# Kernel tuning notes

Hardware: AMD Instinct MI355X
Metric: run time of the kernel (lower is better)

The kernel has to match this reference:

```python
import jax, jax.numpy as jnp
import numpy as np

B = 4096
D_IN = 1024
HIDDEN = [1024, 512, 256]
NUM_DOMAINS = 8


def _glorot(key, shape):
    fan_in, fan_out = shape[-2], shape[-1]
    std = np.sqrt(2.0 / (fan_in + fan_out)).astype(np.float32)
    return jax.random.normal(key, shape, dtype=jnp.float32) * std


def setup_inputs() -> dict:
    key = jax.random.key(0)
    keys = jax.random.split(key, 16)
    dims = [D_IN] + HIDDEN  # per-layer (in, out) = (dims[i], dims[i+1])
    inp = {
        "x": jax.random.normal(keys[0], (B, D_IN), dtype=jnp.float32),
        "indicator": jax.random.randint(keys[1], (B,), 0, NUM_DOMAINS, dtype=jnp.int32),
    }
    for i in range(len(HIDDEN)):
        inp[f"sk{i}"] = _glorot(keys[2 + i], (dims[i], dims[i + 1]))
        inp[f"sb{i}"] = jnp.zeros((dims[i + 1],), dtype=jnp.float32)
        # per-domain kernels stacked on leading domain axis: (D, in, out)
        inp[f"dk{i}"] = _glorot(keys[6 + i], (NUM_DOMAINS, dims[i], dims[i + 1]))
        inp[f"db{i}"] = jnp.zeros((NUM_DOMAINS, dims[i + 1]), dtype=jnp.float32)
    return inp


def reference(x, indicator, sk0, sb0, dk0, db0, sk1, sb1, dk1, db1, sk2, sb2, dk2, db2):
    shared_k = [sk0, sk1, sk2]
    shared_b = [sb0, sb1, sb2]
    domain_k = [dk0, dk1, dk2]
    domain_b = [db0, db1, db2]
    D = dk0.shape[0]
    # Replicate input across all domains: [B, D, d_in] (source computes every domain stack)
    h = jnp.broadcast_to(x[:, None, :], (x.shape[0], D, x.shape[1]))
    for sk, sb, dk, db in zip(shared_k, shared_b, domain_k, domain_b):
        w_eff = sk[None, :, :] * dk          # [D, in, out]  fused shared*domain weights
        b_eff = sb[None, :] + db             # [D, out]
        h = jnp.einsum('bdi,dio->bdo', h, w_eff) + b_eff[None, :, :]
        h = jax.nn.relu(h)                   # all layers use 'relu' (no output_activation)
    one_hot = jax.nn.one_hot(indicator, D, dtype=h.dtype)  # [B, D]
    return jnp.einsum('bdo,bd->bo', h, one_hot)
```

## Files before the change

kernel.cpp:

```cpp
#include <hip/hip_runtime.h>

#define NROWS 4096
#define NDOM 8

typedef short short8 __attribute__((ext_vector_type(8)));
typedef float floatx4 __attribute__((ext_vector_type(4)));
typedef unsigned short ushort4v __attribute__((ext_vector_type(4)));
typedef unsigned short ushort8v __attribute__((ext_vector_type(8)));

__device__ __forceinline__ unsigned short f2bf(float f) {
    union { float f; unsigned u; } v; v.f = f;
    unsigned r = v.u + 0x7FFFu + ((v.u >> 16) & 1u);
    return (unsigned short)(r >> 16);
}

__device__ __forceinline__ void dma16(const void* g, void* l) {
    __builtin_amdgcn_global_load_lds(
        (const __attribute__((address_space(1))) unsigned*)g,
        (__attribute__((address_space(3))) unsigned*)l, 16, 0, 0);
}

__global__ void bucket_kernel(const int* __restrict__ ind,
                              int* __restrict__ offsets,
                              int* __restrict__ rowidx) {
    __shared__ unsigned short cnt[256][NDOM];
    __shared__ int base[256][NDOM];
    __shared__ int dom_total[NDOM];
    __shared__ int dom_off[NDOM + 1];
    const int t = threadIdx.x;

    int myind[16];
#pragma unroll
    for (int i = 0; i < 16; ++i) myind[i] = ind[t * 16 + i];

    unsigned short c[NDOM];
#pragma unroll
    for (int d = 0; d < NDOM; ++d) c[d] = 0;
#pragma unroll
    for (int i = 0; i < 16; ++i) c[myind[i]]++;
#pragma unroll
    for (int d = 0; d < NDOM; ++d) cnt[t][d] = c[d];
    __syncthreads();

    if (t < NDOM) {
        int acc = 0;
        for (int ch = 0; ch < 256; ++ch) { base[ch][t] = acc; acc += cnt[ch][t]; }
        dom_total[t] = acc;
    }
    __syncthreads();
    if (t == 0) {
        int acc = 0;
        for (int d = 0; d < NDOM; ++d) { dom_off[d] = acc; acc += dom_total[d]; }
        dom_off[NDOM] = acc;
    }
    __syncthreads();

    int pos[NDOM];
#pragma unroll
    for (int d = 0; d < NDOM; ++d) pos[d] = dom_off[d] + base[t][d];
#pragma unroll
    for (int i = 0; i < 16; ++i) {
        int dm = myind[i];
        rowidx[pos[dm]++] = t * 16 + i;
    }
    if (t <= NDOM) offsets[t] = dom_off[t];
}

template <int K, int N>
__device__ __forceinline__ void weff_tile(const float* __restrict__ sk,
                                          const float* __restrict__ dk,
                                          unsigned short* __restrict__ wt,
                                          int local) {
    const int d = local & 7;
    const int rest = local >> 3;
    const int k0 = (rest % (K / 64)) * 64;
    const int n0 = (rest / (K / 64)) * 64;
    const int t = threadIdx.x;
    const int n = n0 + (t & 63);
    const int koff = k0 + (t >> 6) * 16;
    unsigned short wb[16];
#pragma unroll
    for (int kk = 0; kk < 16; ++kk) {
        int k = koff + kk;
        float s = sk[(size_t)k * N + n];
        float dd = dk[((size_t)d * K + k) * N + n];
        wb[kk] = f2bf(s * dd);
    }
    unsigned short* dst = wt + ((size_t)d * N + n) * K + koff;
    *(ushort8v*)dst = *(ushort8v*)wb;
    *(ushort8v*)(dst + 8) = *(ushort8v*)(wb + 8);
}

__global__ void precompute_kernel(const float* __restrict__ x,
                                  const int* __restrict__ rowidx,
                                  const float* __restrict__ sk0, const float* __restrict__ dk0,
                                  const float* __restrict__ sk1, const float* __restrict__ dk1,
                                  const float* __restrict__ sk2, const float* __restrict__ dk2,
                                  unsigned short* __restrict__ xb,
                                  unsigned short* __restrict__ w0t,
                                  unsigned short* __restrict__ w1t,
                                  unsigned short* __restrict__ w2t) {
    const int b = blockIdx.x;
    if (b < 256) {
        const int t = threadIdx.x;
#pragma unroll
        for (int r = 0; r < 16; ++r) {
            int p = b * 16 + r;
            int src = rowidx[p];
            floatx4 v = *(const floatx4*)(x + (size_t)src * 1024 + t * 4);
            ushort4v o;
            o[0] = f2bf(v[0]); o[1] = f2bf(v[1]); o[2] = f2bf(v[2]); o[3] = f2bf(v[3]);
            *(ushort4v*)(xb + (size_t)p * 1024 + t * 4) = o;
        }
    } else if (b < 256 + 2048) {
        weff_tile<1024, 1024>(sk0, dk0, w0t, b - 256);
    } else if (b < 256 + 2048 + 1024) {
        weff_tile<1024, 512>(sk1, dk1, w1t, b - (256 + 2048));
    } else {
        weff_tile<512, 256>(sk2, dk2, w2t, b - (256 + 2048 + 1024));
    }
}

template <int FM, int FN, int MSLOTS, int K, int N, bool SCATTER>
__launch_bounds__(256)
__global__ void star_gemm(const unsigned short* __restrict__ Ab,
                          const unsigned short* __restrict__ Wt,
                          const float* __restrict__ sb,
                          const float* __restrict__ db,
                          float* __restrict__ OutF,
                          unsigned short* __restrict__ OutB,
                          const int* __restrict__ offsets,
                          const int* __restrict__ rowidx) {
    constexpr int BM = 32 * FM;
    constexpr int BN = 32 * FN;
    constexpr int NK = K / 64;
    constexpr int AI = BM / 32;
    constexpr int WI = BN / 32;

    __shared__ __align__(128) unsigned short As[BM * 64];
    __shared__ __align__(128) unsigned short Ws[BN * 64];

    const int gid = blockIdx.x;
    const int d = gid & 7;
    const int mslot = (gid >> 3) % MSLOTS;
    const int n0 = (gid / (8 * MSLOTS)) * BN;

    const int bstart = offsets[d];
    const int bend = offsets[d + 1];
    const int bsize = bend - bstart;

    const int tid = threadIdx.x;
    const int lane = tid & 63;
    const int w = tid >> 6;
    const int wy = w >> 1;
    const int wx = w & 1;
    const int lm = lane & 15;
    const int quad = lane >> 4;

    const int lrow = lane >> 3;
    const int phys = lane & 7;

    float bias[FN];
#pragma unroll
    for (int j = 0; j < FN; ++j) {
        int n = n0 + wx * FN * 16 + j * 16 + lm;
        bias[j] = sb[n] + db[d * N + n];
    }

    const unsigned short* wsrc[WI];
    unsigned short* wdst[WI];
#pragma unroll
    for (int j = 0; j < WI; ++j) {
        int nr0 = (w * WI + j) * 8;
        int nn = nr0 + lrow;
        int ch = phys ^ (nn & 7);
        wsrc[j] = Wt + ((size_t)d * N + n0 + nn) * K + ch * 8;
        wdst[j] = Ws + nr0 * 64;
    }

    for (int mt = mslot; mt * BM < bsize; mt += MSLOTS) {
        const int row_start = bstart + mt * BM;

        const unsigned short* asrc[AI];
        unsigned short* adst[AI];
#pragma unroll
        for (int j = 0; j < AI; ++j) {
            int m0 = (w * AI + j) * 8;
            int mm = m0 + lrow;
            int ch = phys ^ (mm & 7);
            int p = row_start + mm; if (p >= bend) p = bend - 1;
            asrc[j] = Ab + (size_t)p * K + ch * 8;
            adst[j] = As + m0 * 64;
        }

        floatx4 acc[FM][FN];
#pragma unroll
        for (int i = 0; i < FM; ++i)
#pragma unroll
            for (int j = 0; j < FN; ++j) acc[i][j] = floatx4{0.f, 0.f, 0.f, 0.f};

        for (int kt = 0; kt < NK; ++kt) {
            const int k0 = kt * 64;
            __syncthreads();
#pragma unroll
            for (int j = 0; j < AI; ++j) dma16(asrc[j] + k0, adst[j]);
#pragma unroll
            for (int j = 0; j < WI; ++j) dma16(wsrc[j] + k0, wdst[j]);
            __syncthreads();
#pragma unroll
            for (int kk = 0; kk < 2; ++kk) {
                short8 av[FM], wv[FN];
#pragma unroll
                for (int i = 0; i < FM; ++i) {
                    int m = wy * FM * 16 + i * 16 + lm;
                    int pc = (kk * 4 + quad) ^ (m & 7);
                    av[i] = *(const short8*)&As[m * 64 + pc * 8];
                }
#pragma unroll
                for (int j = 0; j < FN; ++j) {
                    int n = wx * FN * 16 + j * 16 + lm;
                    int pc = (kk * 4 + quad) ^ (n & 7);
                    wv[j] = *(const short8*)&Ws[n * 64 + pc * 8];
                }
#pragma unroll
                for (int i = 0; i < FM; ++i)
#pragma unroll
                    for (int j = 0; j < FN; ++j)
                        acc[i][j] = __builtin_amdgcn_mfma_f32_16x16x32_bf16(
                            av[i], wv[j], acc[i][j], 0, 0, 0);
            }
        }

#pragma unroll
        for (int i = 0; i < FM; ++i) {
#pragma unroll
            for (int rg = 0; rg < 4; ++rg) {
                int m = wy * FM * 16 + i * 16 + quad * 4 + rg;
                int p = row_start + m;
                if (p < bend) {
                    if constexpr (SCATTER) {
                        int orow = rowidx[p];
#pragma unroll
                        for (int j = 0; j < FN; ++j) {
                            int n = n0 + wx * FN * 16 + j * 16 + lm;
                            float v = acc[i][j][rg] + bias[j];
                            OutF[(size_t)orow * N + n] = v > 0.f ? v : 0.f;
                        }
                    } else {
#pragma unroll
                        for (int j = 0; j < FN; ++j) {
                            int n = n0 + wx * FN * 16 + j * 16 + lm;
                            float v = acc[i][j][rg] + bias[j];
                            OutB[(size_t)p * N + n] = f2bf(v > 0.f ? v : 0.f);
                        }
                    }
                }
            }
        }
    }
}

extern "C" void kernel_launch(void* const* d_in, const int* in_sizes, int n_in,
                              void* d_out, int out_size, void* d_ws, size_t ws_size,
                              hipStream_t stream) {
    const float* x = (const float*)d_in[0];
    const int* ind = (const int*)d_in[1];
    const float* sk0 = (const float*)d_in[2];
    const float* sb0 = (const float*)d_in[3];
    const float* dk0 = (const float*)d_in[4];
    const float* db0 = (const float*)d_in[5];
    const float* sk1 = (const float*)d_in[6];
    const float* sb1 = (const float*)d_in[7];
    const float* dk1 = (const float*)d_in[8];
    const float* db1 = (const float*)d_in[9];
    const float* sk2 = (const float*)d_in[10];
    const float* sb2 = (const float*)d_in[11];
    const float* dk2 = (const float*)d_in[12];
    const float* db2 = (const float*)d_in[13];
    float* out = (float*)d_out;

    char* ws = (char*)d_ws;
    int* offsets = (int*)ws;
    int* rowidx = (int*)(ws + 256);
    unsigned short* xb  = (unsigned short*)(ws + 32768);
    unsigned short* h1  = xb + (size_t)NROWS * 1024;
    unsigned short* h2  = h1 + (size_t)NROWS * 1024;
    unsigned short* w0t = h2 + (size_t)NROWS * 512;
    unsigned short* w1t = w0t + (size_t)NDOM * 1024 * 1024;
    unsigned short* w2t = w1t + (size_t)NDOM * 512 * 1024;

    bucket_kernel<<<1, 256, 0, stream>>>(ind, offsets, rowidx);
    precompute_kernel<<<256 + 2048 + 1024 + 256, 256, 0, stream>>>(
        x, rowidx, sk0, dk0, sk1, dk1, sk2, dk2, xb, w0t, w1t, w2t);

    star_gemm<2, 2, 8, 1024, 1024, false><<<1024, 256, 0, stream>>>(
        xb, w0t, sb0, db0, nullptr, h1, offsets, rowidx);
    star_gemm<2, 2, 8, 1024, 512, false><<<512, 256, 0, stream>>>(
        h1, w1t, sb1, db1, nullptr, h2, offsets, rowidx);
    star_gemm<1, 2, 16, 512, 256, true><<<512, 256, 0, stream>>>(
        h2, w2t, sb2, db2, out, nullptr, offsets, rowidx);
}
```

Before: 206.3 us.

## Fuse bucketing into precompute, gather in first GEMM, double-buffer K tiles

The bucketing kernel is merged into the precompute kernel as an extra block, so one launch is removed. The x cast no longer waits on rowidx because the first GEMM gathers A rows through rowidx instead. The weight-transpose tiles are enlarged and staged through LDS so the global stores become coalesced. The GEMM main loop gains double-buffered LDS with prefetch of the next K tile during MFMA, which doubles LDS use and may lower occupancy.

```diff
diff --git a/kernel.cpp b/kernel.cpp
--- a/kernel.cpp
+++ b/kernel.cpp
@@ -5,7 +5,6 @@
 
 typedef short short8 __attribute__((ext_vector_type(8)));
 typedef float floatx4 __attribute__((ext_vector_type(4)));
-typedef unsigned short ushort4v __attribute__((ext_vector_type(4)));
 typedef unsigned short ushort8v __attribute__((ext_vector_type(8)));
 
 __device__ __forceinline__ unsigned short f2bf(float f) {
@@ -20,108 +19,124 @@
         (__attribute__((address_space(3))) unsigned*)l, 16, 0, 0);
 }
 
-__global__ void bucket_kernel(const int* __restrict__ ind,
-                              int* __restrict__ offsets,
-                              int* __restrict__ rowidx) {
-    __shared__ unsigned short cnt[256][NDOM];
-    __shared__ int base[256][NDOM];
-    __shared__ int dom_total[NDOM];
-    __shared__ int dom_off[NDOM + 1];
-    const int t = threadIdx.x;
-
-    int myind[16];
-#pragma unroll
-    for (int i = 0; i < 16; ++i) myind[i] = ind[t * 16 + i];
-
-    unsigned short c[NDOM];
-#pragma unroll
-    for (int d = 0; d < NDOM; ++d) c[d] = 0;
-#pragma unroll
-    for (int i = 0; i < 16; ++i) c[myind[i]]++;
-#pragma unroll
-    for (int d = 0; d < NDOM; ++d) cnt[t][d] = c[d];
-    __syncthreads();
-
-    if (t < NDOM) {
-        int acc = 0;
-        for (int ch = 0; ch < 256; ++ch) { base[ch][t] = acc; acc += cnt[ch][t]; }
-        dom_total[t] = acc;
-    }
-    __syncthreads();
-    if (t == 0) {
-        int acc = 0;
-        for (int d = 0; d < NDOM; ++d) { dom_off[d] = acc; acc += dom_total[d]; }
-        dom_off[NDOM] = acc;
-    }
-    __syncthreads();
-
-    int pos[NDOM];
-#pragma unroll
-    for (int d = 0; d < NDOM; ++d) pos[d] = dom_off[d] + base[t][d];
-#pragma unroll
-    for (int i = 0; i < 16; ++i) {
-        int dm = myind[i];
-        rowidx[pos[dm]++] = t * 16 + i;
-    }
-    if (t <= NDOM) offsets[t] = dom_off[t];
-}
 
 template <int K, int N>
 __device__ __forceinline__ void weff_tile(const float* __restrict__ sk,
                                           const float* __restrict__ dk,
                                           unsigned short* __restrict__ wt,
+                                          unsigned short* __restrict__ lds,
                                           int local) {
     const int d = local & 7;
     const int rest = local >> 3;
-    const int k0 = (rest % (K / 64)) * 64;
-    const int n0 = (rest / (K / 64)) * 64;
+    const int k0 = (rest & (K / 256 - 1)) * 256;
+    const int n0 = (rest / (K / 256)) * 64;
     const int t = threadIdx.x;
-    const int n = n0 + (t & 63);
-    const int koff = k0 + (t >> 6) * 16;
-    unsigned short wb[16];
-#pragma unroll
-    for (int kk = 0; kk < 16; ++kk) {
-        int k = koff + kk;
-        float s = sk[(size_t)k * N + n];
-        float dd = dk[((size_t)d * K + k) * N + n];
-        wb[kk] = f2bf(s * dd);
-    }
-    unsigned short* dst = wt + ((size_t)d * N + n) * K + koff;
-    *(ushort8v*)dst = *(ushort8v*)wb;
-    *(ushort8v*)(dst + 8) = *(ushort8v*)(wb + 8);
+
+    const int n = t & 63;
+    const int kg = (t >> 6) * 64;
+#pragma unroll
+    for (int c8 = 0; c8 < 8; ++c8) {
+        const int kb = k0 + kg + c8 * 8;
+        unsigned short wb[8];
+#pragma unroll
+        for (int i = 0; i < 8; ++i) {
+            int k = kb + i;
+            wb[i] = f2bf(sk[(size_t)k * N + n0 + n] * dk[((size_t)d * K + k) * N + n0 + n]);
+        }
+        int ch = (kg + c8 * 8) >> 3;
+        int phys = ch ^ (n & 31);
+        *(ushort8v*)&lds[n * 256 + phys * 8] = *(ushort8v*)wb;
+    }
+    __syncthreads();
+
+#pragma unroll
+    for (int it = 0; it < 4; ++it) {
+        const int nn = (t >> 4) + it * 16;
+        const int c = t & 15;
+        ushort8v a = *(ushort8v*)&lds[nn * 256 + ((2 * c) ^ (nn & 31)) * 8];
+        ushort8v b = *(ushort8v*)&lds[nn * 256 + ((2 * c + 1) ^ (nn & 31)) * 8];
+        unsigned short* dst = wt + ((size_t)d * N + n0 + nn) * K + k0 + c * 16;
+        *(ushort8v*)dst = a;
+        *(ushort8v*)(dst + 8) = b;
+    }
 }
 
 __global__ void precompute_kernel(const float* __restrict__ x,
-                                  const int* __restrict__ rowidx,
+                                  const int* __restrict__ ind,
                                   const float* __restrict__ sk0, const float* __restrict__ dk0,
                                   const float* __restrict__ sk1, const float* __restrict__ dk1,
                                   const float* __restrict__ sk2, const float* __restrict__ dk2,
                                   unsigned short* __restrict__ xb,
                                   unsigned short* __restrict__ w0t,
                                   unsigned short* __restrict__ w1t,
-                                  unsigned short* __restrict__ w2t) {
+                                  unsigned short* __restrict__ w2t,
+                                  int* __restrict__ offsets,
+                                  int* __restrict__ rowidx) {
+    __shared__ unsigned short wtile[64 * 256];
+    __shared__ unsigned short cnt[256][NDOM];
+    __shared__ int base[256][NDOM];
+    __shared__ int dom_total[NDOM];
+    __shared__ int dom_off[NDOM + 1];
+
     const int b = blockIdx.x;
+    const int t = threadIdx.x;
+
     if (b < 256) {
-        const int t = threadIdx.x;
-#pragma unroll
-        for (int r = 0; r < 16; ++r) {
-            int p = b * 16 + r;
-            int src = rowidx[p];
-            floatx4 v = *(const floatx4*)(x + (size_t)src * 1024 + t * 4);
-            ushort4v o;
-            o[0] = f2bf(v[0]); o[1] = f2bf(v[1]); o[2] = f2bf(v[2]); o[3] = f2bf(v[3]);
-            *(ushort4v*)(xb + (size_t)p * 1024 + t * 4) = o;
-        }
-    } else if (b < 256 + 2048) {
-        weff_tile<1024, 1024>(sk0, dk0, w0t, b - 256);
-    } else if (b < 256 + 2048 + 1024) {
-        weff_tile<1024, 512>(sk1, dk1, w1t, b - (256 + 2048));
+#pragma unroll
+        for (int pass = 0; pass < 8; ++pass) {
+            int row = b * 16 + pass * 2 + (t >> 7);
+            int ch = t & 127;
+            const float* src = x + (size_t)row * 1024 + ch * 8;
+            floatx4 v0 = *(const floatx4*)src;
+            floatx4 v1 = *(const floatx4*)(src + 4);
+            unsigned short o[8];
+            o[0] = f2bf(v0[0]); o[1] = f2bf(v0[1]); o[2] = f2bf(v0[2]); o[3] = f2bf(v0[3]);
+            o[4] = f2bf(v1[0]); o[5] = f2bf(v1[1]); o[6] = f2bf(v1[2]); o[7] = f2bf(v1[3]);
+            *(ushort8v*)(xb + (size_t)row * 1024 + ch * 8) = *(ushort8v*)o;
+        }
+    } else if (b < 256 + 512) {
+        weff_tile<1024, 1024>(sk0, dk0, w0t, wtile, b - 256);
+    } else if (b < 256 + 512 + 256) {
+        weff_tile<1024, 512>(sk1, dk1, w1t, wtile, b - (256 + 512));
+    } else if (b < 256 + 512 + 256 + 64) {
+        weff_tile<512, 256>(sk2, dk2, w2t, wtile, b - (256 + 512 + 256));
     } else {
-        weff_tile<512, 256>(sk2, dk2, w2t, b - (256 + 2048 + 1024));
-    }
-}
-
-template <int FM, int FN, int MSLOTS, int K, int N, bool SCATTER>
+        int myind[16];
+#pragma unroll
+        for (int i = 0; i < 16; ++i) myind[i] = ind[t * 16 + i];
+        unsigned short c[NDOM];
+#pragma unroll
+        for (int d = 0; d < NDOM; ++d) c[d] = 0;
+#pragma unroll
+        for (int i = 0; i < 16; ++i) c[myind[i]]++;
+#pragma unroll
+        for (int d = 0; d < NDOM; ++d) cnt[t][d] = c[d];
+        __syncthreads();
+        if (t < NDOM) {
+            int acc = 0;
+            for (int ch = 0; ch < 256; ++ch) { base[ch][t] = acc; acc += cnt[ch][t]; }
+            dom_total[t] = acc;
+        }
+        __syncthreads();
+        if (t == 0) {
+            int acc = 0;
+            for (int d = 0; d < NDOM; ++d) { dom_off[d] = acc; acc += dom_total[d]; }
+            dom_off[NDOM] = acc;
+        }
+        __syncthreads();
+        int pos[NDOM];
+#pragma unroll
+        for (int d = 0; d < NDOM; ++d) pos[d] = dom_off[d] + base[t][d];
+#pragma unroll
+        for (int i = 0; i < 16; ++i) {
+            int dm = myind[i];
+            rowidx[pos[dm]++] = t * 16 + i;
+        }
+        if (t <= NDOM) offsets[t] = dom_off[t];
+    }
+}
+
+template <int FM, int FN, int MSLOTS, int K, int N, bool GATHER, bool SCATTER>
 __launch_bounds__(256)
 __global__ void star_gemm(const unsigned short* __restrict__ Ab,
                           const unsigned short* __restrict__ Wt,
@@ -137,8 +152,8 @@
     constexpr int AI = BM / 32;
     constexpr int WI = BN / 32;
 
-    __shared__ __align__(128) unsigned short As[BM * 64];
-    __shared__ __align__(128) unsigned short Ws[BN * 64];
+    __shared__ __align__(128) unsigned short As[2][BM * 64];
+    __shared__ __align__(128) unsigned short Ws[2][BN * 64];
 
     const int gid = blockIdx.x;
     const int d = gid & 7;
@@ -168,30 +183,37 @@
     }
 
     const unsigned short* wsrc[WI];
-    unsigned short* wdst[WI];
 #pragma unroll
     for (int j = 0; j < WI; ++j) {
         int nr0 = (w * WI + j) * 8;
         int nn = nr0 + lrow;
         int ch = phys ^ (nn & 7);
         wsrc[j] = Wt + ((size_t)d * N + n0 + nn) * K + ch * 8;
-        wdst[j] = Ws + nr0 * 64;
     }
 
     for (int mt = mslot; mt * BM < bsize; mt += MSLOTS) {
         const int row_start = bstart + mt * BM;
 
         const unsigned short* asrc[AI];
-        unsigned short* adst[AI];
 #pragma unroll
         for (int j = 0; j < AI; ++j) {
             int m0 = (w * AI + j) * 8;
             int mm = m0 + lrow;
             int ch = phys ^ (mm & 7);
             int p = row_start + mm; if (p >= bend) p = bend - 1;
-            asrc[j] = Ab + (size_t)p * K + ch * 8;
-            adst[j] = As + m0 * 64;
-        }
+            int src = GATHER ? rowidx[p] : p;
+            asrc[j] = Ab + (size_t)src * K + ch * 8;
+        }
+
+        auto dma_tiles = [&](int kt, int buf) {
+            const int k0 = kt * 64;
+#pragma unroll
+            for (int j = 0; j < AI; ++j)
+                dma16(asrc[j] + k0, &As[buf][(w * AI + j) * 512]);
+#pragma unroll
+            for (int j = 0; j < WI; ++j)
+                dma16(wsrc[j] + k0, &Ws[buf][(w * WI + j) * 512]);
+        };
 
         floatx4 acc[FM][FN];
 #pragma unroll
@@ -199,36 +221,36 @@
 #pragma unroll
             for (int j = 0; j < FN; ++j) acc[i][j] = floatx4{0.f, 0.f, 0.f, 0.f};
 
+        dma_tiles(0, 0);
         for (int kt = 0; kt < NK; ++kt) {
-            const int k0 = kt * 64;
+            const int buf = kt & 1;
             __syncthreads();
-#pragma unroll
-            for (int j = 0; j < AI; ++j) dma16(asrc[j] + k0, adst[j]);
-#pragma unroll
-            for (int j = 0; j < WI; ++j) dma16(wsrc[j] + k0, wdst[j]);
-            __syncthreads();
+
+            short8 av[2][FM], wv[2][FN];
 #pragma unroll
             for (int kk = 0; kk < 2; ++kk) {
-                short8 av[FM], wv[FN];
 #pragma unroll
                 for (int i = 0; i < FM; ++i) {
                     int m = wy * FM * 16 + i * 16 + lm;
                     int pc = (kk * 4 + quad) ^ (m & 7);
-                    av[i] = *(const short8*)&As[m * 64 + pc * 8];
+                    av[kk][i] = *(const short8*)&As[buf][m * 64 + pc * 8];
                 }
 #pragma unroll
                 for (int j = 0; j < FN; ++j) {
                     int n = wx * FN * 16 + j * 16 + lm;
                     int pc = (kk * 4 + quad) ^ (n & 7);
-                    wv[j] = *(const short8*)&Ws[n * 64 + pc * 8];
+                    wv[kk][j] = *(const short8*)&Ws[buf][n * 64 + pc * 8];
                 }
+            }
+            if (kt + 1 < NK) dma_tiles(kt + 1, 1 - buf);
+#pragma unroll
+            for (int kk = 0; kk < 2; ++kk)
 #pragma unroll
                 for (int i = 0; i < FM; ++i)
 #pragma unroll
                     for (int j = 0; j < FN; ++j)
                         acc[i][j] = __builtin_amdgcn_mfma_f32_16x16x32_bf16(
-                            av[i], wv[j], acc[i][j], 0, 0, 0);
-            }
+                            av[kk][i], wv[kk][j], acc[i][j], 0, 0, 0);
         }
 
 #pragma unroll
@@ -289,14 +311,13 @@
     unsigned short* w1t = w0t + (size_t)NDOM * 1024 * 1024;
     unsigned short* w2t = w1t + (size_t)NDOM * 512 * 1024;
 
-    bucket_kernel<<<1, 256, 0, stream>>>(ind, offsets, rowidx);
-    precompute_kernel<<<256 + 2048 + 1024 + 256, 256, 0, stream>>>(
-        x, rowidx, sk0, dk0, sk1, dk1, sk2, dk2, xb, w0t, w1t, w2t);
-
-    star_gemm<2, 2, 8, 1024, 1024, false><<<1024, 256, 0, stream>>>(
+    precompute_kernel<<<256 + 512 + 256 + 64 + 1, 256, 0, stream>>>(
+        x, ind, sk0, dk0, sk1, dk1, sk2, dk2, xb, w0t, w1t, w2t, offsets, rowidx);
+
+    star_gemm<2, 2, 8, 1024, 1024, true, false><<<1024, 256, 0, stream>>>(
         xb, w0t, sb0, db0, nullptr, h1, offsets, rowidx);
-    star_gemm<2, 2, 8, 1024, 512, false><<<512, 256, 0, stream>>>(
+    star_gemm<2, 2, 8, 1024, 512, false, false><<<512, 256, 0, stream>>>(
         h1, w1t, sb1, db1, nullptr, h2, offsets, rowidx);
-    star_gemm<1, 2, 16, 512, 256, true><<<512, 256, 0, stream>>>(
+    star_gemm<1, 2, 16, 512, 256, false, true><<<512, 256, 0, stream>>>(
         h2, w2t, sb2, db2, out, nullptr, offsets, rowidx);
 }
```

Result: faster. 187.6 us (-9.1%).
